# Kernel tuning notes

Measured on AMD Instinct MI355X. Metric: run time of the kernel, lower is better.

## Reference

```python
import jax, jax.numpy as jnp
import numpy as np
from jax import lax

N, L, K, DROP = 2048, 512, 16, 2
DIM = N - L * DROP  # 1024 father wavelets


def setup_inputs() -> dict:
    key = jax.random.key(0)
    kA, kO = jax.random.split(key)
    A = jax.random.normal(kA, (N, N), dtype=jnp.float32)
    A = 0.5 * (A + A.T)  # symmetric, like a graph Laplacian
    O = jax.random.normal(kO, (L, K, K), dtype=jnp.float32) / np.float32(np.sqrt(K))
    # Index structure faithful to the module: each level selects K indices,
    # DROP of which are freshly-dropped wavelet indices, the rest drawn from
    # the pool of indices that stay active through all L levels.
    rng = np.random.default_rng(0)
    perm = rng.permutation(N)
    dropped = perm[: L * DROP].reshape(L, DROP)
    pool = perm[L * DROP:]  # size DIM, always active
    rest = np.stack([rng.choice(pool, K - DROP, replace=False) for _ in range(L)])
    idx = np.sort(np.concatenate([dropped, rest], axis=1), axis=1).astype(np.int32)
    active_idx = np.sort(pool).astype(np.int32)        # final_active_index == 1
    inactive_idx = np.sort(perm[: L * DROP]).astype(np.int32)  # dropped (mother)
    return {
        "A": A,
        "O": O,
        "idx": jnp.asarray(idx),
        "active_idx": jnp.asarray(active_idx),
        "inactive_idx": jnp.asarray(inactive_idx),
    }


def reference(A, O, idx, active_idx, inactive_idx):
    n = A.shape[0]
    dt = A.dtype

    # Each level's U is identity except the KxK block O at rows/cols idx[l].
    # Hence U @ A @ U^T only rewrites K rows then K cols of A, and U @ right
    # only rewrites K rows of right -- same math as the dense NxN matmuls in
    # the original, expressed as the O(N*K) structured update.
    def step(carry, xs):
        Acur, right = carry
        Ol, il = xs
        Acur = Acur.at[il].set(Ol @ Acur[il])              # rows of U @ A
        Acur = Acur.at[:, il].set(Acur[:, il] @ Ol.T)      # cols of (U@A) @ U^T
        right = right.at[il].set(Ol @ right[il])           # U @ right
        return (Acur, right), None

    right0 = jnp.eye(n, dtype=dt)  # right after l==0 becomes U_0 @ I = U_0
    (A_out, right), _ = lax.scan(step, (A, right0), (O, idx))

    active = jnp.zeros((n,), dt).at[active_idx].set(1.0)
    outer = active[:, None] * active[None, :]
    # left_index = I - diag(diag(outer)) + outer ; diag(outer) == active
    left = jnp.eye(n, dtype=dt) - jnp.diag(active) + outer
    D = A_out * left

    mother_coefficients = D[jnp.ix_(inactive_idx, inactive_idx)]  # (N-dim, N-dim)
    father_coefficients = D[jnp.ix_(active_idx, active_idx)]      # (dim, dim)
    mother_wavelets = right[inactive_idx]                         # (N-dim, N)
    father_wavelets = right[active_idx]                           # (dim, N)
    A_rec = right.T @ D @ right
    return (A_rec, right, D, mother_coefficients, father_coefficients,
            mother_wavelets, father_wavelets)
```

## Files before the change

### kernel.cpp

```cpp
#include <hip/hip_runtime.h>

#define NDIM 2048
#define LLEV 512
#define KDIM 16
#define HALF 1024

typedef __attribute__((ext_vector_type(8))) short bf16x8;
typedef __attribute__((ext_vector_type(4))) float f32x4;

__device__ inline unsigned short f2bf(float x) {
    unsigned u = __float_as_uint(x);
    u += 0x7fffu + ((u >> 16) & 1u);
    return (unsigned short)(u >> 16);
}
__device__ inline float bf2f(unsigned short b) {
    return __uint_as_float(((unsigned)b) << 16);
}
__device__ inline void split2(float x, unsigned short& h, unsigned short& l) {
    h = f2bf(x);
    l = f2bf(x - bf2f(h));
}

__device__ inline void gl2lds16(const void* g, void* l) {
    __builtin_amdgcn_global_load_lds(
        (const __attribute__((address_space(1))) void*)g,
        (__attribute__((address_space(3))) void*)l, 16, 0, 0);
}

__global__ __launch_bounds__(64) void compose_kernel(const float* __restrict__ O,
                                                     const int* __restrict__ idx,
                                                     int* __restrict__ Sarr,
                                                     float* __restrict__ Warr)
{
    __shared__ int s_S[32];
    __shared__ int s_pos[32];
    __shared__ float s_W[32][33];
    const int t = blockIdx.x;
    const int lane = threadIdx.x;
    const int* a = idx + (2 * t) * 16;
    const int* b = idx + (2 * t + 1) * 16;

    if (lane == 0) {
        int na = 0, i = 0, j = 0;
        while (i < 16 || j < 16) {
            int va = (i < 16) ? a[i] : 0x7fffffff;
            int vb = (j < 16) ? b[j] : 0x7fffffff;
            int v = va < vb ? va : vb;
            if (va == v) i++;
            if (vb == v) j++;
            s_S[na++] = v;
        }
        const int nm = na;
        int r = 0, p = 0;
        while (na < 32) {
            while (p < nm && s_S[p] < r) p++;
            if (p < nm && s_S[p] == r) { r++; continue; }
            s_S[na++] = r++;
        }
    }
    __syncthreads();
    if (lane < 32) {
        const int v = (lane < 16) ? a[lane] : b[lane - 16];
        int pp = 0;
        #pragma unroll
        for (int q = 0; q < 32; ++q) if (s_S[q] == v) pp = q;
        s_pos[lane] = pp;
        #pragma unroll
        for (int c = 0; c < 33; ++c) s_W[lane][c] = 0.f;
        s_W[lane][lane] = 1.f;
    }
    __syncthreads();
    const int j  = lane >> 2;
    const int cg = (lane & 3) * 8;
    #pragma unroll
    for (int step = 0; step < 2; ++step) {
        const float* Om = O + (size_t)(2 * t + step) * 256;
        float acc[8] = {};
        for (int k = 0; k < 16; ++k) {
            const float o = Om[j * 16 + k];
            const int p = s_pos[step * 16 + k];
            #pragma unroll
            for (int c = 0; c < 8; ++c) acc[c] += o * s_W[p][cg + c];
        }
        __syncthreads();
        const int pj = s_pos[step * 16 + j];
        #pragma unroll
        for (int c = 0; c < 8; ++c) s_W[pj][cg + c] = acc[c];
        __syncthreads();
    }
    if (lane < 32) Sarr[t * 32 + lane] = s_S[lane];
    {
        const int r = lane >> 1, h0 = (lane & 1) * 16;
        float* wp = Warr + (size_t)t * 1024 + r * 32 + h0;
        #pragma unroll
        for (int c = 0; c < 16; ++c) wp[c] = s_W[r][h0 + c];
    }
}

__global__ __launch_bounds__(64) void scan3_kernel(const float* __restrict__ Warr,
                                                   const int* __restrict__ Sarr,
                                                   float* __restrict__ right)
{
    __shared__ float slab[NDIM * 4];
    const int lane = threadIdx.x;
    const int c0 = blockIdx.x * 4;
    const int rr = lane & 31;
    const int ks = lane >> 5;

    for (int r = lane; r < NDIM; r += 64)
        *(float4*)&slab[r * 4] = make_float4(0.f, 0.f, 0.f, 0.f);
    if (lane < 4) slab[(c0 + lane) * 4 + lane] = 1.0f;

    int rows[16]; float cf[16]; int wrow;
    {
        const int4* sp = (const int4*)(Sarr + ks * 16);
        #pragma unroll
        for (int q = 0; q < 4; ++q) *(int4*)&rows[q * 4] = sp[q];
        const float4* wp = (const float4*)(Warr + rr * 32 + ks * 16);
        #pragma unroll
        for (int q = 0; q < 4; ++q) *(float4*)&cf[q * 4] = wp[q];
        wrow = Sarr[rr];
    }

    for (int t = 0; t < 256; ++t) {
        int cr[16]; float cc[16];
        const int wr = wrow;
        #pragma unroll
        for (int q = 0; q < 16; ++q) { cr[q] = rows[q]; cc[q] = cf[q]; }
        if (t + 1 < 256) {
            const int4* sp = (const int4*)(Sarr + (t + 1) * 32 + ks * 16);
            #pragma unroll
            for (int q = 0; q < 4; ++q) *(int4*)&rows[q * 4] = sp[q];
            const float4* wp = (const float4*)(Warr + (size_t)(t + 1) * 1024 + rr * 32 + ks * 16);
            #pragma unroll
            for (int q = 0; q < 4; ++q) *(float4*)&cf[q * 4] = wp[q];
            wrow = Sarr[(t + 1) * 32 + rr];
        }
        float4 acc = make_float4(0.f, 0.f, 0.f, 0.f);
        #pragma unroll
        for (int j = 0; j < 16; ++j) {
            float4 v = *(const float4*)&slab[cr[j] * 4];
            acc.x += cc[j] * v.x; acc.y += cc[j] * v.y;
            acc.z += cc[j] * v.z; acc.w += cc[j] * v.w;
        }
        acc.x += __shfl_xor(acc.x, 32, 64);
        acc.y += __shfl_xor(acc.y, 32, 64);
        acc.z += __shfl_xor(acc.z, 32, 64);
        acc.w += __shfl_xor(acc.w, 32, 64);
        if (lane < 32)
            *(float4*)&slab[wr * 4] = acc;
    }

    #pragma unroll 4
    for (int i = 0; i < 32; ++i) {
        const int r = i * 64 + lane;
        *(float4*)(right + (size_t)r * NDIM + c0) = *(float4*)&slab[r * 4];
    }
}

__global__ __launch_bounds__(64) void scan_kernel(const float* __restrict__ O,
                                                  const int* __restrict__ idx,
                                                  float* __restrict__ right)
{
    __shared__ float slab[NDIM * 8];
    const int lane = threadIdx.x;
    const int c0 = blockIdx.x * 8;
    const int k  = lane >> 2;
    const int c2 = (lane & 3) * 2;

    for (int r = lane; r < NDIM; r += 64) {
        *(float4*)&slab[r * 8]     = make_float4(0.f, 0.f, 0.f, 0.f);
        *(float4*)&slab[r * 8 + 4] = make_float4(0.f, 0.f, 0.f, 0.f);
    }
    if (lane < 8) slab[(c0 + lane) * 8 + lane] = 1.0f;

    int rows[16]; float a[16]; int wrow;
    #pragma unroll
    for (int j = 0; j < 16; ++j) rows[j] = idx[j];
    {
        const float4* p4 = (const float4*)(O + k * 16);
        #pragma unroll
        for (int q = 0; q < 4; ++q) *(float4*)&a[q * 4] = p4[q];
    }
    wrow = idx[k];

    for (int l = 0; l < LLEV; ++l) {
        int rr[16]; float aa[16];
        const int wr = wrow;
        #pragma unroll
        for (int j = 0; j < 16; ++j) { rr[j] = rows[j]; aa[j] = a[j]; }
        if (l + 1 < LLEV) {
            const int* ip = idx + (l + 1) * 16;
            #pragma unroll
            for (int j = 0; j < 16; ++j) rows[j] = ip[j];
            const float4* p4 = (const float4*)(O + (l + 1) * 256 + k * 16);
            #pragma unroll
            for (int q = 0; q < 4; ++q) *(float4*)&a[q * 4] = p4[q];
            wrow = ip[k];
        }
        float sx = 0.f, sy = 0.f;
        #pragma unroll
        for (int j = 0; j < 16; ++j) {
            float2 v = *(float2*)&slab[rr[j] * 8 + c2];
            sx += aa[j] * v.x;
            sy += aa[j] * v.y;
        }
        *(float2*)&slab[wr * 8 + c2] = make_float2(sx, sy);
    }

    for (int r0 = 0; r0 < NDIM; r0 += 32) {
        const int r = r0 + (lane >> 1);
        const int h = (lane & 1) * 4;
        *(float4*)(right + (size_t)r * NDIM + c0 + h) = *(float4*)&slab[r * 8 + h];
    }
}

#define GBK 64
__global__ __launch_bounds__(256) void mfma_nt(const unsigned short* __restrict__ Ah,
                                               const unsigned short* __restrict__ Al,
                                               const unsigned short* __restrict__ Bh,
                                               const unsigned short* __restrict__ Bl,
                                               float* __restrict__ C,
                                               long strideZ,
                                               int M, int N, int K, int ksplit)
{
    __shared__ unsigned short sA_h[8 * 128 * 8];
    __shared__ unsigned short sA_l[8 * 128 * 8];
    __shared__ unsigned short sB_h[8 * 128 * 8];
    __shared__ unsigned short sB_l[8 * 128 * 8];

    const int tid  = threadIdx.x;
    const int wave = tid >> 6, lane = tid & 63;
    const int lm   = lane & 15, quad = lane >> 4;
    const int wm   = wave & 1,  wn   = wave >> 1;
    const int m0   = blockIdx.x * 128, n0 = blockIdx.y * 128;
    const int Kz   = K / ksplit;
    const int kbeg = Kz * blockIdx.z;
    C += (size_t)blockIdx.z * strideZ;

    const unsigned short* gbase;
    unsigned short* sbase;
    if      (wave == 0) { gbase = Ah + (size_t)m0 * K; sbase = sA_h; }
    else if (wave == 1) { gbase = Al + (size_t)m0 * K; sbase = sA_l; }
    else if (wave == 2) { gbase = Bh + (size_t)n0 * K; sbase = sB_h; }
    else                { gbase = Bl + (size_t)n0 * K; sbase = sB_l; }

    f32x4 acc[4][4];
    #pragma unroll
    for (int i = 0; i < 4; ++i)
        #pragma unroll
        for (int j = 0; j < 4; ++j) acc[i][j] = (f32x4){0.f, 0.f, 0.f, 0.f};

    for (int k0 = kbeg; k0 < kbeg + Kz; k0 += GBK) {
        #pragma unroll
        for (int h = 0; h < 2; ++h) {
            const unsigned short* gr = gbase + (size_t)(h * 64 + lane) * K + k0;
            unsigned short* sb = sbase + h * 512;
            #pragma unroll
            for (int c = 0; c < 8; ++c)
                gl2lds16(gr + c * 8, sb + c * 1024);
        }
        __syncthreads();
        #pragma unroll
        for (int sub = 0; sub < 2; ++sub) {
            const int co = (sub * 4 + quad) * 1024;
            bf16x8 ah[4], al[4], bh[4], bl[4];
            #pragma unroll
            for (int i = 0; i < 4; ++i) {
                const int m = wm * 64 + i * 16 + lm;
                ah[i] = *(const bf16x8*)&sA_h[co + m * 8];
                al[i] = *(const bf16x8*)&sA_l[co + m * 8];
            }
            #pragma unroll
            for (int j = 0; j < 4; ++j) {
                const int n = wn * 64 + j * 16 + lm;
                bh[j] = *(const bf16x8*)&sB_h[co + n * 8];
                bl[j] = *(const bf16x8*)&sB_l[co + n * 8];
            }
            #pragma unroll
            for (int i = 0; i < 4; ++i)
                #pragma unroll
                for (int j = 0; j < 4; ++j) {
                    acc[i][j] = __builtin_amdgcn_mfma_f32_16x16x32_bf16(ah[i], bh[j], acc[i][j], 0, 0, 0);
                    acc[i][j] = __builtin_amdgcn_mfma_f32_16x16x32_bf16(ah[i], bl[j], acc[i][j], 0, 0, 0);
                    acc[i][j] = __builtin_amdgcn_mfma_f32_16x16x32_bf16(al[i], bh[j], acc[i][j], 0, 0, 0);
                }
        }
        __syncthreads();
    }
    #pragma unroll
    for (int i = 0; i < 4; ++i) {
        const int mrow = m0 + wm * 64 + i * 16 + quad * 4;
        #pragma unroll
        for (int j = 0; j < 4; ++j) {
            float* cp = C + (size_t)mrow * N + n0 + wn * 64 + j * 16 + lm;
            #pragma unroll
            for (int r = 0; r < 4; ++r) cp[(size_t)r * N] = acc[i][j][r];
        }
    }
}

__global__ __launch_bounds__(256) void reduce_k(float* __restrict__ dst,
                                                const float* __restrict__ parts,
                                                long strideZ, int nz, long n)
{
    const long i = ((long)blockIdx.x * 256 + threadIdx.x) * 4;
    if (i >= n) return;
    float4 s = *(const float4*)(parts + i);
    for (int z = 1; z < nz; ++z) {
        float4 v = *(const float4*)(parts + (size_t)z * strideZ + i);
        s.x += v.x; s.y += v.y; s.z += v.z; s.w += v.w;
    }
    *(float4*)(dst + i) = s;
}

__global__ __launch_bounds__(256) void conv_hl(const float* __restrict__ src,
                                               const float* __restrict__ src2,
                                               const int* __restrict__ gidx,
                                               int kshift,
                                               unsigned short* __restrict__ h,
                                               unsigned short* __restrict__ l)
{
    const long e = ((long)blockIdx.x * 256 + threadIdx.x) * 4;
    long off;
    if (gidx) {
        const long row = e >> kshift;
        const long col = e - (row << kshift);
        off = ((size_t)gidx[row] << kshift) + col;
    } else {
        off = e;
    }
    float4 v = *(const float4*)(src + off);
    if (src2) {
        float4 v2 = *(const float4*)(src2 + off);
        v.x += v2.x; v.y += v2.y; v.z += v2.z; v.w += v2.w;
    }
    ushort4 hh, ll;
    split2(v.x, hh.x, ll.x); split2(v.y, hh.y, ll.y);
    split2(v.z, hh.z, ll.z); split2(v.w, hh.w, ll.w);
    *(ushort4*)(h + e) = hh;
    *(ushort4*)(l + e) = ll;
}

__global__ __launch_bounds__(512) void gather_conv(const float* __restrict__ R,
                                                   const int* __restrict__ ridx,
                                                   float* __restrict__ outp,
                                                   unsigned short* __restrict__ h,
                                                   unsigned short* __restrict__ l)
{
    const int r = blockIdx.x;
    const int c = threadIdx.x * 4;
    const size_t e = (size_t)r * NDIM + c;
    float4 v = *(const float4*)(R + (size_t)ridx[r] * NDIM + c);
    *(float4*)(outp + e) = v;
    ushort4 hh, ll;
    split2(v.x, hh.x, ll.x); split2(v.y, hh.y, ll.y);
    split2(v.z, hh.z, ll.z); split2(v.w, hh.w, ll.w);
    *(ushort4*)(h + e) = hh;
    *(ushort4*)(l + e) = ll;
}

__global__ __launch_bounds__(256) void tconv_hl(const float* __restrict__ src,
                                                int Msrc, int Ksrc,
                                                unsigned short* __restrict__ h,
                                                unsigned short* __restrict__ l)
{
    __shared__ float t[64][65];
    const int bi = blockIdx.x, bj = blockIdx.y;
    const int tx = threadIdx.x & 15, ty = threadIdx.x >> 4;
    #pragma unroll
    for (int r = 0; r < 4; ++r) {
        const int row = bi * 64 + ty + r * 16;
        float4 v = *(const float4*)(src + (size_t)row * Ksrc + bj * 64 + tx * 4);
        t[ty + r * 16][tx * 4 + 0] = v.x; t[ty + r * 16][tx * 4 + 1] = v.y;
        t[ty + r * 16][tx * 4 + 2] = v.z; t[ty + r * 16][tx * 4 + 3] = v.w;
    }
    __syncthreads();
    #pragma unroll
    for (int r = 0; r < 4; ++r) {
        const int drow = bj * 64 + ty + r * 16;
        ushort4 hh, ll;
        split2(t[tx * 4 + 0][ty + r * 16], hh.x, ll.x);
        split2(t[tx * 4 + 1][ty + r * 16], hh.y, ll.y);
        split2(t[tx * 4 + 2][ty + r * 16], hh.z, ll.z);
        split2(t[tx * 4 + 3][ty + r * 16], hh.w, ll.w);
        *(ushort4*)(h + (size_t)drow * Msrc + bi * 64 + tx * 4) = hh;
        *(ushort4*)(l + (size_t)drow * Msrc + bi * 64 + tx * 4) = ll;
    }
}

__global__ __launch_bounds__(256) void gt_build(const float* __restrict__ W1a,
                                                const float* __restrict__ W1b,
                                                const float* __restrict__ right,
                                                const int* __restrict__ inva,
                                                const float* __restrict__ dmrow,
                                                unsigned short* __restrict__ h,
                                                unsigned short* __restrict__ l)
{
    __shared__ float t[64][65];
    const int bi = blockIdx.x, bj = blockIdx.y;
    const int tx = threadIdx.x & 15, ty = threadIdx.x >> 4;
    #pragma unroll
    for (int rr = 0; rr < 4; ++rr) {
        const int r = bi * 64 + ty + rr * 16;
        const int ia = inva[r];
        float4 v;
        if (ia >= 0) {
            const size_t o = (size_t)ia * NDIM + bj * 64 + tx * 4;
            v = *(const float4*)(W1a + o);
            float4 v2 = *(const float4*)(W1b + o);
            v.x += v2.x; v.y += v2.y; v.z += v2.z; v.w += v2.w;
        } else {
            v = *(const float4*)(right + (size_t)r * NDIM + bj * 64 + tx * 4);
            const float s = dmrow[r];
            v.x *= s; v.y *= s; v.z *= s; v.w *= s;
        }
        t[ty + rr * 16][tx * 4 + 0] = v.x; t[ty + rr * 16][tx * 4 + 1] = v.y;
        t[ty + rr * 16][tx * 4 + 2] = v.z; t[ty + rr * 16][tx * 4 + 3] = v.w;
    }
    __syncthreads();
    #pragma unroll
    for (int rr = 0; rr < 4; ++rr) {
        const int drow = bj * 64 + ty + rr * 16;
        ushort4 hh, ll;
        split2(t[tx * 4 + 0][ty + rr * 16], hh.x, ll.x);
        split2(t[tx * 4 + 1][ty + rr * 16], hh.y, ll.y);
        split2(t[tx * 4 + 2][ty + rr * 16], hh.z, ll.z);
        split2(t[tx * 4 + 3][ty + rr * 16], hh.w, ll.w);
        *(ushort4*)(h + (size_t)drow * NDIM + bi * 64 + tx * 4) = hh;
        *(ushort4*)(l + (size_t)drow * NDIM + bi * 64 + tx * 4) = ll;
    }
}

__global__ __launch_bounds__(256) void diag_kernel(const float* __restrict__ P,
                                                   const float* __restrict__ P2,
                                                   const float* __restrict__ R,
                                                   float* __restrict__ diag_all)
{
    __shared__ float red[256];
    const int i = blockIdx.x;
    const float4* p4 = (const float4*)(P + (size_t)i * NDIM);
    const float4* q4 = P2 ? (const float4*)(P2 + (size_t)i * NDIM) : nullptr;
    const float4* r4 = (const float4*)(R + (size_t)i * NDIM);
    float s = 0.f;
    for (int kq = threadIdx.x; kq < NDIM / 4; kq += 256) {
        float4 a = p4[kq], b = r4[kq];
        if (q4) {
            float4 a2 = q4[kq];
            a.x += a2.x; a.y += a2.y; a.z += a2.z; a.w += a2.w;
        }
        s += a.x * b.x + a.y * b.y + a.z * b.z + a.w * b.w;
    }
    red[threadIdx.x] = s;
    __syncthreads();
    for (int off = 128; off > 0; off >>= 1) {
        if (threadIdx.x < off) red[threadIdx.x] += red[threadIdx.x + off];
        __syncthreads();
    }
    if (threadIdx.x == 0) diag_all[i] = red[0];
}

__global__ void prep2_kernel(const int* __restrict__ act, const int* __restrict__ inact,
                             const float* __restrict__ diag_all,
                             int* __restrict__ inva, float* __restrict__ dm,
                             float* __restrict__ dmrow)
{
    const int t = threadIdx.x;
    inva[t] = -1;
    inva[t + HALF] = -1;
    __syncthreads();
    inva[act[t]] = t;
    const int ir = inact[t];
    const float dv = diag_all[ir];
    dm[t] = dv;
    dmrow[ir] = dv;
}

__global__ __launch_bounds__(256) void build_D(const float* __restrict__ Daa,
                                               const float* __restrict__ diag_all,
                                               const int* __restrict__ inva,
                                               float* __restrict__ D)
{
    const int e = blockIdx.x * 256 + threadIdx.x;
    const int i = e >> 11, j = e & (NDIM - 1);
    const int ii = inva[i], jj = inva[j];
    float v = 0.f;
    if (ii >= 0 && jj >= 0) v = Daa[ii * HALF + jj];
    if (i == j) v = diag_all[i];
    D[e] = v;
}

__global__ __launch_bounds__(256) void mc_kernel(const float* __restrict__ dm,
                                                 float* __restrict__ mc)
{
    const int e = blockIdx.x * 256 + threadIdx.x;
    const int t = e >> 10, s = e & (HALF - 1);
    mc[e] = (t == s) ? dm[t] : 0.f;
}

__global__ __launch_bounds__(512) void gather_rows(const float* __restrict__ R,
                                                   const int* __restrict__ ridx,
                                                   float* __restrict__ outp)
{
    const int r = blockIdx.x;
    const int c = threadIdx.x * 4;
    *(float4*)(outp + (size_t)r * NDIM + c) =
        *(const float4*)(R + (size_t)ridx[r] * NDIM + c);
}

__global__ __launch_bounds__(256) void gemm_nt64(const float* __restrict__ A, int lda,
                                                 const int* __restrict__ ridxA,
                                                 const float* __restrict__ B, int ldb,
                                                 const int* __restrict__ ridxB,
                                                 float* __restrict__ C, int ldc, int Kk)
{
    __shared__ float As[16][68];
    __shared__ float Bs[16][68];
    const int tid = threadIdx.x;
    const int tx = tid & 15, ty = tid >> 4;
    const int m0 = blockIdx.x * 64, n0 = blockIdx.y * 64;
    const int li = tid >> 2;
    const int lk = (tid & 3) * 4;
    int rowA = m0 + li; if (ridxA) rowA = ridxA[rowA];
    int rowB = n0 + li; if (ridxB) rowB = ridxB[rowB];
    const float* pA = A + (size_t)rowA * lda + lk;
    const float* pB = B + (size_t)rowB * ldb + lk;
    float acc[4][4] = {};
    for (int k0 = 0; k0 < Kk; k0 += 16) {
        float4 a4 = *(const float4*)(pA + k0);
        float4 b4 = *(const float4*)(pB + k0);
        As[lk + 0][li] = a4.x; As[lk + 1][li] = a4.y; As[lk + 2][li] = a4.z; As[lk + 3][li] = a4.w;
        Bs[lk + 0][li] = b4.x; Bs[lk + 1][li] = b4.y; Bs[lk + 2][li] = b4.z; Bs[lk + 3][li] = b4.w;
        __syncthreads();
        #pragma unroll
        for (int kk = 0; kk < 16; ++kk) {
            float4 av = *(const float4*)&As[kk][ty * 4];
            float4 bv = *(const float4*)&Bs[kk][tx * 4];
            float a[4] = {av.x, av.y, av.z, av.w};
            float b[4] = {bv.x, bv.y, bv.z, bv.w};
            #pragma unroll
            for (int i = 0; i < 4; ++i)
                #pragma unroll
                for (int j = 0; j < 4; ++j) acc[i][j] += a[i] * b[j];
        }
        __syncthreads();
    }
    #pragma unroll
    for (int i = 0; i < 4; ++i) {
        float4 v = make_float4(acc[i][0], acc[i][1], acc[i][2], acc[i][3]);
        *(float4*)(C + (size_t)(m0 + ty * 4 + i) * ldc + n0 + tx * 4) = v;
    }
}

__global__ __launch_bounds__(256) void gemm_nn64(const float* __restrict__ A, int lda,
                                                 const float* __restrict__ B, int ldb,
                                                 float* __restrict__ C, int ldc, int Kk)
{
    __shared__ float As[16][68];
    __shared__ float Bs[16][68];
    const int tid = threadIdx.x;
    const int tx = tid & 15, ty = tid >> 4;
    const int m0 = blockIdx.x * 64, n0 = blockIdx.y * 64;
    const int li = tid >> 2;
    const int lk = (tid & 3) * 4;
    const int bk = tid >> 4;
    const int bn = (tid & 15) * 4;
    const float* pA = A + (size_t)(m0 + li) * lda + lk;
    float acc[4][4] = {};
    for (int k0 = 0; k0 < Kk; k0 += 16) {
        float4 a4 = *(const float4*)(pA + k0);
        float4 b4 = *(const float4*)(B + (size_t)(k0 + bk) * ldb + n0 + bn);
        As[lk + 0][li] = a4.x; As[lk + 1][li] = a4.y; As[lk + 2][li] = a4.z; As[lk + 3][li] = a4.w;
        *(float4*)&Bs[bk][bn] = b4;
        __syncthreads();
        #pragma unroll
        for (int kk = 0; kk < 16; ++kk) {
            float4 av = *(const float4*)&As[kk][ty * 4];
            float4 bv = *(const float4*)&Bs[kk][tx * 4];
            float a[4] = {av.x, av.y, av.z, av.w};
            float b[4] = {bv.x, bv.y, bv.z, bv.w};
            #pragma unroll
            for (int i = 0; i < 4; ++i)
                #pragma unroll
                for (int j = 0; j < 4; ++j) acc[i][j] += a[i] * b[j];
        }
        __syncthreads();
    }
    #pragma unroll
    for (int i = 0; i < 4; ++i) {
        float4 v = make_float4(acc[i][0], acc[i][1], acc[i][2], acc[i][3]);
        *(float4*)(C + (size_t)(m0 + ty * 4 + i) * ldc + n0 + tx * 4) = v;
    }
}

__global__ __launch_bounds__(256) void arec64(const float* __restrict__ fw,
                                              const float* __restrict__ mw,
                                              const float* __restrict__ W1,
                                              const float* __restrict__ dm,
                                              float* __restrict__ C)
{
    __shared__ float As[16][68];
    __shared__ float Bs[16][68];
    const int tid = threadIdx.x;
    const int tx = tid & 15, ty = tid >> 4;
    const int m0 = blockIdx.x * 64, n0 = blockIdx.y * 64;
    const int bk = tid >> 4;
    const int bn = (tid & 15) * 4;
    float acc[4][4] = {};
    for (int t0 = 0; t0 < NDIM; t0 += 16) {
        const int t = t0 + bk;
        const float* Hrow; const float* Grow; float gs;
        if (t < HALF) { Hrow = fw + (size_t)t * NDIM; Grow = W1 + (size_t)t * NDIM; gs = 1.f; }
        else          { Hrow = mw + (size_t)(t - HALF) * NDIM; Grow = Hrow; gs = dm[t - HALF]; }
        float4 a4 = *(const float4*)(Hrow + m0 + bn);
        float4 b4 = *(const float4*)(Grow + n0 + bn);
        b4.x *= gs; b4.y *= gs; b4.z *= gs; b4.w *= gs;
        *(float4*)&As[bk][bn] = a4;
        *(float4*)&Bs[bk][bn] = b4;
        __syncthreads();
        #pragma unroll
        for (int kk = 0; kk < 16; ++kk) {
            float4 av = *(const float4*)&As[kk][ty * 4];
            float4 bv = *(const float4*)&Bs[kk][tx * 4];
            float a[4] = {av.x, av.y, av.z, av.w};
            float b[4] = {bv.x, bv.y, bv.z, bv.w};
            #pragma unroll
            for (int i = 0; i < 4; ++i)
                #pragma unroll
                for (int j = 0; j < 4; ++j) acc[i][j] += a[i] * b[j];
        }
        __syncthreads();
    }
    #pragma unroll
    for (int i = 0; i < 4; ++i) {
        float4 v = make_float4(acc[i][0], acc[i][1], acc[i][2], acc[i][3]);
        *(float4*)(C + (size_t)(m0 + ty * 4 + i) * NDIM + n0 + tx * 4) = v;
    }
}

extern "C" void kernel_launch(void* const* d_in, const int* in_sizes, int n_in,
                              void* d_out, int out_size, void* d_ws, size_t ws_size,
                              hipStream_t stream)
{
    (void)in_sizes; (void)n_in; (void)out_size;
    const float* A     = (const float*)d_in[0];
    const float* O     = (const float*)d_in[1];
    const int*   idx   = (const int*)d_in[2];
    const int*   act   = (const int*)d_in[3];
    const int*   inact = (const int*)d_in[4];

    float* out = (float*)d_out;
    const size_t NN = (size_t)NDIM * NDIM;
    float* A_rec = out;
    float* right = out + NN;
    float* D     = out + 2 * NN;
    float* mc    = out + 3 * NN;
    float* fc    = mc + (size_t)HALF * HALF;
    float* mw    = fc + (size_t)HALF * HALF;
    float* fw    = mw + (size_t)HALF * NDIM;

    char*  w        = (char*)d_ws;
    float* diag_all = (float*)w;
    float* dm       = (float*)(w + 8192);
    int*   inva     = (int*)(w + 12288);
    float* dmrow    = (float*)(w + 20480);

    const size_t MB = 1024 * 1024;
    const size_t WS_NEEDED = 65536 + 32 * MB;

    if (ws_size >= WS_NEEDED) {
        char* r1 = w + 65536;
        char* r2 = r1 + 16 * MB;
        float* Warr = (float*)r1;
        int*   Sarr = (int*)(r1 + MB);
        unsigned short* Rh  = (unsigned short*)r1;
        unsigned short* Rl  = (unsigned short*)(r1 + 8 * MB);
        unsigned short* RTh = Rh;
        unsigned short* RTl = Rl;
        unsigned short* Ah  = (unsigned short*)r2;
        unsigned short* Al  = (unsigned short*)(r2 + 8 * MB);
        unsigned short* Pah = (unsigned short*)r2;
        unsigned short* Pal = (unsigned short*)(r2 + 4 * MB);
        unsigned short* Fh  = (unsigned short*)(r2 + 8 * MB);
        unsigned short* Fl  = (unsigned short*)(r2 + 12 * MB);
        unsigned short* Dh  = (unsigned short*)r2;
        unsigned short* Dl  = (unsigned short*)(r2 + 2 * MB);
        unsigned short* FTh = (unsigned short*)(r2 + 4 * MB);
        unsigned short* FTl = (unsigned short*)(r2 + 8 * MB);
        unsigned short* GTh = (unsigned short*)r2;
        unsigned short* GTl = (unsigned short*)(r2 + 8 * MB);

        compose_kernel<<<256, 64, 0, stream>>>(O, idx, Sarr, Warr);
        scan3_kernel<<<512, 64, 0, stream>>>(Warr, Sarr, right);
        gather_rows<<<1024, 512, 0, stream>>>(right, inact, mw);
        conv_hl<<<4096, 256, 0, stream>>>(right, nullptr, nullptr, 11, Rh, Rl);
        conv_hl<<<4096, 256, 0, stream>>>(A, nullptr, nullptr, 11, Ah, Al);
        mfma_nt<<<dim3(16, 16, 2), 256, 0, stream>>>(Rh, Rl, Ah, Al, A_rec,
                                                     (long)2 * NN, NDIM, NDIM, NDIM, 2);
        diag_kernel<<<2048, 256, 0, stream>>>(A_rec, A_rec + 2 * NN, right, diag_all);
        prep2_kernel<<<1, 1024, 0, stream>>>(act, inact, diag_all, inva, dm, dmrow);
        conv_hl<<<2048, 256, 0, stream>>>(A_rec, A_rec + 2 * NN, act, 11, Pah, Pal);
        gather_conv<<<1024, 512, 0, stream>>>(right, act, fw, Fh, Fl);
        mfma_nt<<<dim3(8, 8, 4), 256, 0, stream>>>(Pah, Pal, Fh, Fl, D,
                                                   (long)HALF * HALF, HALF, HALF, NDIM, 4);
        reduce_k<<<1024, 256, 0, stream>>>(fc, D, (long)HALF * HALF, 4, (long)HALF * HALF);
        conv_hl<<<1024, 256, 0, stream>>>(fc, nullptr, nullptr, 10, Dh, Dl);
        tconv_hl<<<dim3(16, 32), 256, 0, stream>>>(fw, HALF, NDIM, FTh, FTl);
        mfma_nt<<<dim3(8, 16, 2), 256, 0, stream>>>(Dh, Dl, FTh, FTl, D,
                                                    (long)HALF * NDIM, HALF, NDIM, HALF, 2);
        tconv_hl<<<dim3(32, 32), 256, 0, stream>>>(right, NDIM, NDIM, RTh, RTl);
        gt_build<<<dim3(32, 32), 256, 0, stream>>>(D, D + (size_t)HALF * NDIM,
                                                   right, inva, dmrow, GTh, GTl);
        mfma_nt<<<dim3(16, 16, 2), 256, 0, stream>>>(RTh, RTl, GTh, GTl, A_rec,
                                                     (long)2 * NN, NDIM, NDIM, NDIM, 2);
        reduce_k<<<4096, 256, 0, stream>>>(A_rec, A_rec, (long)2 * NN, 2, (long)NN);
        build_D<<<16384, 256, 0, stream>>>(fc, diag_all, inva, D);
        mc_kernel<<<4096, 256, 0, stream>>>(dm, mc);
    } else {
        scan_kernel<<<256, 64, 0, stream>>>(O, idx, right);
        gather_rows<<<1024, 512, 0, stream>>>(right, act, fw);
        gather_rows<<<1024, 512, 0, stream>>>(right, inact, mw);
        gemm_nt64<<<dim3(32, 32), 256, 0, stream>>>(right, NDIM, nullptr, A, NDIM, nullptr,
                                                    A_rec, NDIM, NDIM);
        diag_kernel<<<2048, 256, 0, stream>>>(A_rec, nullptr, right, diag_all);
        prep2_kernel<<<1, 1024, 0, stream>>>(act, inact, diag_all, inva, dm, dmrow);
        gemm_nt64<<<dim3(16, 16), 256, 0, stream>>>(A_rec, NDIM, act, right, NDIM, act,
                                                    fc, HALF, NDIM);
        gemm_nn64<<<dim3(16, 32), 256, 0, stream>>>(fc, HALF, fw, NDIM, D, NDIM, HALF);
        arec64<<<dim3(32, 32), 256, 0, stream>>>(fw, mw, D, dm, A_rec);
        build_D<<<16384, 256, 0, stream>>>(fc, diag_all, inva, D);
        mc_kernel<<<4096, 256, 0, stream>>>(dm, mc);
    }
}
```

Baseline: 559.0 us.

## Fuse A bf16 split into scan kernel and halve GEMM K-tile

The fp32-to-bf16 hi/lo split of A now runs as extra blocks of the scan kernel, so it overlaps the scan's low-occupancy work and one launch is removed. The mfma_nt GEMM K-tile is also halved from 64 to 32, cutting LDS use per block, which may raise occupancy but doubles the number of barrier and load rounds. The mixed-role scan blocks still declare the large shared slab, so the conversion blocks may have limited residency.

```diff
diff --git a/kernel.cpp b/kernel.cpp
--- a/kernel.cpp
+++ b/kernel.cpp
@@ -97,12 +97,32 @@
     }
 }
 
-__global__ __launch_bounds__(64) void scan3_kernel(const float* __restrict__ Warr,
-                                                   const int* __restrict__ Sarr,
-                                                   float* __restrict__ right)
+__global__ __launch_bounds__(64) void scan3_fused(const float* __restrict__ Warr,
+                                                  const int* __restrict__ Sarr,
+                                                  float* __restrict__ right,
+                                                  const float* __restrict__ Asrc,
+                                                  unsigned short* __restrict__ Ahd,
+                                                  unsigned short* __restrict__ Ald)
 {
     __shared__ float slab[NDIM * 4];
     const int lane = threadIdx.x;
+
+    if (blockIdx.x >= 512) {
+        const long e = ((long)(blockIdx.x - 512) * 64 + lane) * 8;
+        float4 v0 = *(const float4*)(Asrc + e);
+        float4 v1 = *(const float4*)(Asrc + e + 4);
+        ushort4 h0, l0, h1, l1;
+        split2(v0.x, h0.x, l0.x); split2(v0.y, h0.y, l0.y);
+        split2(v0.z, h0.z, l0.z); split2(v0.w, h0.w, l0.w);
+        split2(v1.x, h1.x, l1.x); split2(v1.y, h1.y, l1.y);
+        split2(v1.z, h1.z, l1.z); split2(v1.w, h1.w, l1.w);
+        *(ushort4*)(Ahd + e)     = h0;
+        *(ushort4*)(Ahd + e + 4) = h1;
+        *(ushort4*)(Ald + e)     = l0;
+        *(ushort4*)(Ald + e + 4) = l1;
+        return;
+    }
+
     const int c0 = blockIdx.x * 4;
     const int rr = lane & 31;
     const int ks = lane >> 5;
@@ -215,7 +235,7 @@
     }
 }
 
-#define GBK 64
+#define GBK 32
 __global__ __launch_bounds__(256) void mfma_nt(const unsigned short* __restrict__ Ah,
                                                const unsigned short* __restrict__ Al,
                                                const unsigned short* __restrict__ Bh,
@@ -224,10 +244,10 @@
                                                long strideZ,
                                                int M, int N, int K, int ksplit)
 {
-    __shared__ unsigned short sA_h[8 * 128 * 8];
-    __shared__ unsigned short sA_l[8 * 128 * 8];
-    __shared__ unsigned short sB_h[8 * 128 * 8];
-    __shared__ unsigned short sB_l[8 * 128 * 8];
+    __shared__ unsigned short sA_h[4 * 128 * 8];
+    __shared__ unsigned short sA_l[4 * 128 * 8];
+    __shared__ unsigned short sB_h[4 * 128 * 8];
+    __shared__ unsigned short sB_l[4 * 128 * 8];
 
     const int tid  = threadIdx.x;
     const int wave = tid >> 6, lane = tid & 63;
@@ -257,13 +277,12 @@
             const unsigned short* gr = gbase + (size_t)(h * 64 + lane) * K + k0;
             unsigned short* sb = sbase + h * 512;
             #pragma unroll
-            for (int c = 0; c < 8; ++c)
+            for (int c = 0; c < 4; ++c)
                 gl2lds16(gr + c * 8, sb + c * 1024);
         }
         __syncthreads();
-        #pragma unroll
-        for (int sub = 0; sub < 2; ++sub) {
-            const int co = (sub * 4 + quad) * 1024;
+        {
+            const int co = quad * 1024;
             bf16x8 ah[4], al[4], bh[4], bl[4];
             #pragma unroll
             for (int i = 0; i < 4; ++i) {
@@ -691,10 +710,9 @@
         unsigned short* GTl = (unsigned short*)(r2 + 8 * MB);
 
         compose_kernel<<<256, 64, 0, stream>>>(O, idx, Sarr, Warr);
-        scan3_kernel<<<512, 64, 0, stream>>>(Warr, Sarr, right);
+        scan3_fused<<<512 + 8192, 64, 0, stream>>>(Warr, Sarr, right, A, Ah, Al);
         gather_rows<<<1024, 512, 0, stream>>>(right, inact, mw);
         conv_hl<<<4096, 256, 0, stream>>>(right, nullptr, nullptr, 11, Rh, Rl);
-        conv_hl<<<4096, 256, 0, stream>>>(A, nullptr, nullptr, 11, Ah, Al);
         mfma_nt<<<dim3(16, 16, 2), 256, 0, stream>>>(Rh, Rl, Ah, Al, A_rec,
                                                      (long)2 * NN, NDIM, NDIM, NDIM, 2);
         diag_kernel<<<2048, 256, 0, stream>>>(A_rec, A_rec + 2 * NN, right, diag_all);
```

After: 540.2 us. 3.4% less time.
